# Kernel optimization log

Hardware: AMD Instinct MI355X
Metric: run time of the kernel (lower is better)

The kernel has to match this reference:

```python
import jax, jax.numpy as jnp
import numpy as np

B, S, DIM = 2, 2048, 4096
HQ, HKV, HD = 32, 8, 128
N_REP = HQ // HKV
MAX_S = 2048
ROPE_BASE = 10000.0


def rotate_half(x):
    half = x.shape[-1] // 2
    return jnp.concatenate([-x[..., half:], x[..., :half]], axis=-1)


def setup_inputs() -> dict:
    key = jax.random.key(0)
    ks = jax.random.split(key, 8)
    x = jax.random.normal(ks[0], (B, S, DIM), dtype=jnp.float32)
    Wq = jax.random.normal(ks[1], (HQ * HD, DIM), dtype=jnp.float32) * 0.02
    bq = jax.random.normal(ks[2], (HQ * HD,), dtype=jnp.float32) * 0.02
    Wk = jax.random.normal(ks[3], (HKV * HD, DIM), dtype=jnp.float32) * 0.02
    bk = jax.random.normal(ks[4], (HKV * HD,), dtype=jnp.float32) * 0.02
    Wv = jax.random.normal(ks[5], (HKV * HD, DIM), dtype=jnp.float32) * 0.02
    bv = jax.random.normal(ks[6], (HKV * HD,), dtype=jnp.float32) * 0.02
    Wo = jax.random.normal(ks[7], (DIM, HQ * HD), dtype=jnp.float32) * 0.02
    # RoPE tables (HF convention: angles duplicated across both halves)
    inv_freq = 1.0 / (ROPE_BASE ** (jnp.arange(0, HD, 2, dtype=jnp.float32) / HD))
    pos = jnp.arange(S, dtype=jnp.float32)
    ang = pos[:, None] * inv_freq[None, :]              # [S, HD/2]
    emb = jnp.concatenate([ang, ang], axis=-1)          # [S, HD]
    cos, sin = jnp.cos(emb), jnp.sin(emb)
    # static KV cache, zero-initialized as in the module
    cache_k = jnp.zeros((B, HKV, MAX_S, HD), dtype=jnp.float32)
    cache_v = jnp.zeros((B, HKV, MAX_S, HD), dtype=jnp.float32)
    # causal additive mask
    causal = jnp.tril(jnp.ones((S, S), dtype=bool))
    mask = jnp.where(causal, 0.0, -1e9).astype(jnp.float32)[None, None]  # [1,1,S,S]
    return {"x": x, "cos": cos, "sin": sin, "Wq": Wq, "bq": bq, "Wk": Wk,
            "bk": bk, "Wv": Wv, "bv": bv, "Wo": Wo, "cache_k": cache_k,
            "cache_v": cache_v, "mask": mask, "start_pos": 0}


def reference(x, cos, sin, Wq, bq, Wk, bk, Wv, bv, Wo, cache_k, cache_v, mask, start_pos):
    bsz, seqlen, _ = x.shape
    scaling = 1.0 / jnp.sqrt(jnp.float32(HD))
    # QKV projections
    xq = (jnp.einsum('bsd,ed->bse', x, Wq) + bq).reshape(bsz, seqlen, HQ, HD).transpose(0, 2, 1, 3)
    xk = (jnp.einsum('bsd,ed->bse', x, Wk) + bk).reshape(bsz, seqlen, HKV, HD).transpose(0, 2, 1, 3)
    xv = (jnp.einsum('bsd,ed->bse', x, Wv) + bv).reshape(bsz, seqlen, HKV, HD).transpose(0, 2, 1, 3)
    # RoPE
    c = cos[None, None]  # [1,1,S,HD]
    s = sin[None, None]
    xq = xq * c + rotate_half(xq) * s
    xk = xk * c + rotate_half(xk) * s
    # static KV-cache append + slice (start_pos is a Python int)
    cache_k = jax.lax.dynamic_update_slice(cache_k, xk, (0, 0, start_pos, 0))
    cache_v = jax.lax.dynamic_update_slice(cache_v, xv, (0, 0, start_pos, 0))
    keys = cache_k[:, :, :start_pos + seqlen]     # [B,HKV,K,HD]
    values = cache_v[:, :, :start_pos + seqlen]
    # GQA: repeat kv heads (repeat_interleave over head dim)
    keys = jnp.repeat(keys, N_REP, axis=1)        # [B,HQ,K,HD]
    values = jnp.repeat(values, N_REP, axis=1)
    # SDPA with additive mask
    scores = jnp.einsum('bhqd,bhkd->bhqk', xq, keys) * scaling + mask
    attn = jax.nn.softmax(scores, axis=-1)
    out = jnp.einsum('bhqk,bhkd->bhqd', attn, values)
    out = out.transpose(0, 2, 1, 3).reshape(bsz, seqlen, HQ * HD)
    return jnp.einsum('bse,de->bsd', out, Wo)
```

## Files before the change

### kernel.cpp

```cpp
#include <hip/hip_runtime.h>

typedef _Float16 half8 __attribute__((ext_vector_type(8)));
typedef _Float16 half4 __attribute__((ext_vector_type(4)));
typedef float floatx4 __attribute__((ext_vector_type(4)));
typedef float floatx16 __attribute__((ext_vector_type(16)));

#define SWZ(r) ((((r) & 7) << 1) | (((r) >> 3) & 1))

__device__ __forceinline__ void gld16(const void* g, void* l) {
  __builtin_amdgcn_global_load_lds(
      (const __attribute__((address_space(1))) unsigned int*)g,
      (__attribute__((address_space(3))) unsigned int*)l, 16, 0, 0);
}

__global__ void convert_all(const float* __restrict__ x, const float* __restrict__ Wq,
                            const float* __restrict__ Wk, const float* __restrict__ Wv,
                            const float* __restrict__ Wo, const float* __restrict__ bq,
                            const float* __restrict__ bk, const float* __restrict__ bv,
                            _Float16* __restrict__ xb, _Float16* __restrict__ wqkv,
                            _Float16* __restrict__ wo_b, float* __restrict__ biasc) {
  long i = (long)blockIdx.x * 256 + threadIdx.x;
  const long N0 = 2097152, N1 = N0 + 2097152, N2 = N1 + 524288, N3 = N2 + 524288,
             N4 = N3 + 2097152;
  const float* s;
  _Float16* d;
  long j;
  if (i < N0) { s = x; d = xb; j = i; }
  else if (i < N1) { s = Wq; d = wqkv; j = i - N0; }
  else if (i < N2) { s = Wk; d = wqkv + (size_t)4096 * 4096; j = i - N1; }
  else if (i < N3) { s = Wv; d = wqkv + (size_t)5120 * 4096; j = i - N2; }
  else if (i < N4) { s = Wo; d = wo_b; j = i - N3; }
  else {
    long k = i - N4;
    if (k < 4096) biasc[k] = bq[k];
    else if (k < 5120) biasc[k] = bk[k - 4096];
    else if (k < 6144) biasc[k] = bv[k - 5120];
    return;
  }
  float4 a = ((const float4*)s)[2 * j];
  float4 b2 = ((const float4*)s)[2 * j + 1];
  half8 h;
  h[0] = (_Float16)a.x; h[1] = (_Float16)a.y; h[2] = (_Float16)a.z; h[3] = (_Float16)a.w;
  h[4] = (_Float16)b2.x; h[5] = (_Float16)b2.y; h[6] = (_Float16)b2.z; h[7] = (_Float16)b2.w;
  ((half8*)d)[j] = h;
}

template <typename OutT, bool HasBias>
__global__ __launch_bounds__(256) void gemm_bt(const _Float16* __restrict__ A,
                                               const _Float16* __restrict__ B,
                                               const float* __restrict__ bias,
                                               OutT* __restrict__ C, int M, int N, int K) {
  __shared__ _Float16 as[128 * 64];
  __shared__ _Float16 bs[128 * 64];
  const int tid = threadIdx.x;
  const int w = tid >> 6, lane = tid & 63;
  const int quad = lane >> 4, l16 = lane & 15;
  const int M0 = blockIdx.y * 128, N0 = blockIdx.x * 128;
  const int wm = (w >> 1) * 64, wn = (w & 1) * 64;

  floatx4 acc[4][4];
#pragma unroll
  for (int i = 0; i < 4; ++i)
#pragma unroll
    for (int j = 0; j < 4; ++j) acc[i][j] = (floatx4){0.f, 0.f, 0.f, 0.f};

  const int sr = tid >> 3, g0 = tid & 7;
  const int csw = (g0 ^ (sr & 7)) * 8;
  const _Float16* Ag[4];
  const _Float16* Bg[4];
  _Float16* asd[4];
  _Float16* bsd[4];
#pragma unroll
  for (int c = 0; c < 4; ++c) {
    Ag[c] = A + (size_t)(M0 + c * 32 + sr) * K + csw;
    Bg[c] = B + (size_t)(N0 + c * 32 + sr) * K + csw;
    asd[c] = &as[(c * 32 + w * 8) * 64];
    bsd[c] = &bs[(c * 32 + w * 8) * 64];
  }

  int aoff[4][2], boff[4][2];
#pragma unroll
  for (int mi = 0; mi < 4; ++mi)
#pragma unroll
    for (int kd = 0; kd < 2; ++kd) {
      int ra = wm + mi * 16 + l16;
      aoff[mi][kd] = ra * 64 + (((kd * 4 + quad) ^ (ra & 7)) * 8);
      int rb = wn + mi * 16 + l16;
      boff[mi][kd] = rb * 64 + (((kd * 4 + quad) ^ (rb & 7)) * 8);
    }

  for (int kk = 0; kk < K; kk += 64) {
    __syncthreads();
#pragma unroll
    for (int c = 0; c < 4; ++c) gld16(Ag[c] + kk, asd[c]);
#pragma unroll
    for (int c = 0; c < 4; ++c) gld16(Bg[c] + kk, bsd[c]);
    __syncthreads();
#pragma unroll
    for (int kd = 0; kd < 2; ++kd) {
      half8 af[4], bf[4];
#pragma unroll
      for (int i = 0; i < 4; ++i) af[i] = *(const half8*)&as[aoff[i][kd]];
#pragma unroll
      for (int i = 0; i < 4; ++i) bf[i] = *(const half8*)&bs[boff[i][kd]];
#pragma unroll
      for (int mi = 0; mi < 4; ++mi)
#pragma unroll
        for (int ni = 0; ni < 4; ++ni)
          acc[mi][ni] = __builtin_amdgcn_mfma_f32_16x16x32_f16(af[mi], bf[ni], acc[mi][ni], 0, 0, 0);
    }
  }

#pragma unroll
  for (int mi = 0; mi < 4; ++mi)
#pragma unroll
    for (int ni = 0; ni < 4; ++ni) {
      int row = M0 + wm + mi * 16 + quad * 4;
      int col = N0 + wn + ni * 16 + l16;
      float bvv = HasBias ? bias[col] : 0.f;
#pragma unroll
      for (int r = 0; r < 4; ++r) {
        float v = acc[mi][ni][r] + bvv;
        C[(size_t)(row + r) * N + col] = (OutT)v;
      }
    }
}

template <typename OutT, bool HasBias>
__global__ __launch_bounds__(512, 2) void gemm256(const _Float16* __restrict__ A,
                                                  const _Float16* __restrict__ B,
                                                  const float* __restrict__ bias,
                                                  OutT* __restrict__ C, int M, int N, int K) {
  __shared__ _Float16 as[2][256 * 64];
  __shared__ _Float16 bs[2][256 * 64];
  const int tid = threadIdx.x;
  const int w = tid >> 6, lane = tid & 63;
  const int quad = lane >> 4, l16 = lane & 15;
  const int sw7 = l16 & 7;
  const int M0 = blockIdx.y * 256, N0 = blockIdx.x * 256;
  const int wm = (w >> 2) * 128, wn = (w & 3) * 64;
  const int NT = K >> 6;

  floatx4 acc[8][4];
#pragma unroll
  for (int i = 0; i < 8; ++i)
#pragma unroll
    for (int j = 0; j < 4; ++j) acc[i][j] = (floatx4){0.f, 0.f, 0.f, 0.f};

  const int sr = tid >> 3;
  const int csw = ((tid & 7) ^ (sr & 7)) * 8;
  const _Float16* Ag[4];
  const _Float16* Bg[4];
#pragma unroll
  for (int j = 0; j < 4; ++j) {
    Ag[j] = A + (size_t)(M0 + j * 64 + sr) * K + csw;
    Bg[j] = B + (size_t)(N0 + j * 64 + sr) * K + csw;
  }

#define STA(p, t, j) gld16(Ag[j] + (size_t)(t) * 64, &as[p][(j) * 4096 + w * 512])
#define STB(p, t, j) gld16(Bg[j] + (size_t)(t) * 64, &bs[p][(j) * 4096 + w * 512])

#define FRA(p, q, mi, kd) \
  (*(const half8*)&as[p][(wm + (q) * 32 + (mi) * 16 + l16) * 64 + ((((kd) * 4 + quad) ^ sw7) * 8)])
#define FRB(p, ni, kd) \
  (*(const half8*)&bs[p][(wn + (ni) * 16 + l16) * 64 + ((((kd) * 4 + quad) ^ sw7) * 8)])

#define LD_A(p, q)                                   \
  _Pragma("unroll") for (int kd = 0; kd < 2; ++kd)   \
  _Pragma("unroll") for (int mi = 0; mi < 2; ++mi)   \
      af[mi][kd] = FRA(p, q, mi, kd);

#define LD_B(p)                                      \
  _Pragma("unroll") for (int kd = 0; kd < 2; ++kd)   \
  _Pragma("unroll") for (int ni = 0; ni < 4; ++ni)   \
      bf[ni][kd] = FRB(p, ni, kd);

#define PH_COMPUTE(q)                                                                  \
  __builtin_amdgcn_s_barrier();                                                        \
  asm volatile("s_waitcnt lgkmcnt(0)" ::: "memory");                                   \
  __builtin_amdgcn_sched_barrier(0);                                                   \
  __builtin_amdgcn_s_setprio(1);                                                       \
  _Pragma("unroll") for (int kd = 0; kd < 2; ++kd)                                     \
  _Pragma("unroll") for (int mi = 0; mi < 2; ++mi)                                     \
  _Pragma("unroll") for (int ni = 0; ni < 4; ++ni)                                     \
      acc[(q) * 2 + mi][ni] = __builtin_amdgcn_mfma_f32_16x16x32_f16(                  \
          af[mi][kd], bf[ni][kd], acc[(q) * 2 + mi][ni], 0, 0, 0);                     \
  __builtin_amdgcn_s_setprio(0);

  half8 bf[4][2], af[2][2];

  STA(0, 0, 0); STA(0, 0, 1); STA(0, 0, 2); STA(0, 0, 3);
  STB(0, 0, 0); STB(0, 0, 1); STB(0, 0, 2); STB(0, 0, 3);
  STB(1, 1, 0); STB(1, 1, 1); STB(1, 1, 2); STB(1, 1, 3);
  asm volatile("s_waitcnt vmcnt(4)" ::: "memory");
  __builtin_amdgcn_s_barrier();

  for (int t = 0; t < NT; t += 2) {
    const int t2 = (t + 2 < NT) ? t + 2 : t;
    const int t3 = (t + 3 < NT) ? t + 3 : t + 1;

    LD_B(0); LD_A(0, 0);
    STA(1, t + 1, 0); STA(1, t + 1, 1); STA(1, t + 1, 2); STA(1, t + 1, 3);
    PH_COMPUTE(0);
    __builtin_amdgcn_s_barrier();

    LD_A(0, 1);
    STB(0, t2, 0); STB(0, t2, 1);
    PH_COMPUTE(1);
    __builtin_amdgcn_s_barrier();

    LD_A(0, 2);
    STB(0, t2, 2); STB(0, t2, 3);
    PH_COMPUTE(2);
    __builtin_amdgcn_s_barrier();

    LD_A(0, 3);
    PH_COMPUTE(3);
    asm volatile("s_waitcnt vmcnt(4)" ::: "memory");
    __builtin_amdgcn_sched_barrier(0);
    __builtin_amdgcn_s_barrier();

    LD_B(1); LD_A(1, 0);
    STA(0, t2, 0); STA(0, t2, 1);
    PH_COMPUTE(0);
    __builtin_amdgcn_s_barrier();

    LD_A(1, 1);
    STA(0, t2, 2); STA(0, t2, 3);
    PH_COMPUTE(1);
    __builtin_amdgcn_s_barrier();

    LD_A(1, 2);
    STB(1, t3, 0); STB(1, t3, 1);
    PH_COMPUTE(2);
    __builtin_amdgcn_s_barrier();

    LD_A(1, 3);
    STB(1, t3, 2); STB(1, t3, 3);
    PH_COMPUTE(3);
    asm volatile("s_waitcnt vmcnt(4)" ::: "memory");
    __builtin_amdgcn_sched_barrier(0);
    __builtin_amdgcn_s_barrier();
  }
  asm volatile("s_waitcnt vmcnt(0)" ::: "memory");

#pragma unroll
  for (int mf = 0; mf < 8; ++mf)
#pragma unroll
    for (int ni = 0; ni < 4; ++ni) {
      int row = M0 + wm + mf * 16 + quad * 4;
      int col = N0 + wn + ni * 16 + l16;
      float bvv = HasBias ? bias[col] : 0.f;
#pragma unroll
      for (int r = 0; r < 4; ++r) C[(size_t)(row + r) * N + col] = (OutT)(acc[mf][ni][r] + bvv);
    }
#undef STA
#undef STB
#undef FRA
#undef FRB
#undef LD_A
#undef LD_B
#undef PH_COMPUTE
}

__global__ void rope_qk(const _Float16* __restrict__ qkv, const float* __restrict__ cosb,
                        const float* __restrict__ sinb, _Float16* __restrict__ q_r,
                        _Float16* __restrict__ k_r) {
  int t = blockIdx.x * 256 + threadIdx.x;
  int d = t & 63;
  int r = t >> 6;
  int hh = r % 40;
  int r2 = r / 40;
  int s = r2 & 2047;
  int b = r2 >> 11;
  size_t mrow = (size_t)(b * 2048 + s) * 6144;
  float c = cosb[s * 128 + d], sn = sinb[s * 128 + d];
  if (hh < 32) {
    size_t base = mrow + hh * 128 + d;
    float x1 = (float)qkv[base], x2 = (float)qkv[base + 64];
    const float sc = 0.12751744737079736f;
    float o1 = (x1 * c - x2 * sn) * sc;
    float o2 = (x2 * c + x1 * sn) * sc;
    size_t ob = ((size_t)((b * 32 + hh) * 2048 + s)) * 128 + d;
    q_r[ob] = (_Float16)o1;
    q_r[ob + 64] = (_Float16)o2;
  } else {
    int hk = hh - 32;
    size_t base = mrow + 4096 + hk * 128 + d;
    float x1 = (float)qkv[base], x2 = (float)qkv[base + 64];
    float o1 = x1 * c - x2 * sn;
    float o2 = x2 * c + x1 * sn;
    size_t ob = ((size_t)((b * 8 + hk) * 2048 + s)) * 128 + d;
    k_r[ob] = (_Float16)o1;
    k_r[ob + 64] = (_Float16)o2;
  }
}

__global__ void v_transpose(const _Float16* __restrict__ qkv, _Float16* __restrict__ v_t) {
  __shared__ _Float16 tile[32][33];
  int st = blockIdx.x * 32, dt = blockIdx.y * 32, bh = blockIdx.z;
  int tx = threadIdx.x & 31, ty = threadIdx.x >> 5;
  int b = bh >> 3, hv = bh & 7;
#pragma unroll
  for (int j = 0; j < 4; ++j) {
    int s = st + ty + j * 8;
    tile[ty + j * 8][tx] = qkv[(size_t)(b * 2048 + s) * 6144 + 5120 + hv * 128 + dt + tx];
  }
  __syncthreads();
#pragma unroll
  for (int j = 0; j < 4; ++j)
    v_t[((size_t)bh * 128 + dt + ty + j * 8) * 2048 + st + tx] = tile[tx][ty + j * 8];
}

__global__ __launch_bounds__(256, 2) void attn_kernel(const _Float16* __restrict__ q_r,
                                                      const _Float16* __restrict__ k_r,
                                                      const _Float16* __restrict__ v_t,
                                                      _Float16* __restrict__ att) {
  __shared__ __align__(16) _Float16 kbuf[2][64 * 128];
  __shared__ __align__(16) _Float16 vbuf[2][128 * 64];
  const int tid = threadIdx.x;
  const int w = tid >> 6, lane = tid & 63;
  const int l32 = lane & 31, hi = lane >> 5;
  const int qb = 15 - blockIdx.x;
  const int h = blockIdx.y, b = blockIdx.z;
  const int q0 = qb * 128;
  const _Float16* qh = q_r + ((size_t)(b * 32 + h) * 2048) * 128;
  const _Float16* kh = k_r + ((size_t)(b * 8 + (h >> 2)) * 2048) * 128;
  const _Float16* vh = v_t + ((size_t)(b * 8 + (h >> 2)) * 128) * 2048;

  const int ql = w * 32 + l32;
  const int myq = q0 + ql;
  const int swq7 = ql & 7;
  const int swl = SWZ(l32);

  half8 bq[8];
#pragma unroll
  for (int kd = 0; kd < 8; ++kd)
    bq[kd] = *(const half8*)&qh[(size_t)myq * 128 + kd * 16 + hi * 8];

  floatx16 oacc[4];
#pragma unroll
  for (int di = 0; di < 4; ++di)
#pragma unroll
    for (int j = 0; j < 16; ++j) oacc[di][j] = 0.f;
  float mrun = -1e30f, lrun = 0.f;

  const int krow = tid >> 4, kgrp = tid & 15;
  const int vrow = tid >> 3, vgrp = tid & 7;

#define STAGE_KV(p, t)                                                                     \
  do {                                                                                     \
    const _Float16* kg_ = kh + (size_t)(t) * 64 * 128;                                     \
    _Pragma("unroll") for (int c = 0; c < 4; ++c) {                                        \
      int row = c * 16 + krow;                                                             \
      gld16(kg_ + row * 128 + ((kgrp ^ SWZ(row)) * 8), &kbuf[p][(c * 16 + w * 4) * 128]);  \
    }                                                                                      \
    _Pragma("unroll") for (int c = 0; c < 4; ++c) {                                        \
      int row = c * 32 + vrow;                                                             \
      gld16(vh + (size_t)row * 2048 + (size_t)(t) * 64 + ((vgrp ^ (row & 7)) * 8),         \
            &vbuf[p][(c * 32 + w * 8) * 64]);                                              \
    }                                                                                      \
  } while (0)

  const int nsteps = 2 * qb + 2;
  STAGE_KV(0, 0);

  for (int s = 0; s < nsteps; ++s) {
    const int cur = s & 1;
    __syncthreads();
    const int sn = (s + 1 < nsteps) ? s + 1 : s;
    STAGE_KV(cur ^ 1, sn);
    asm volatile("s_waitcnt vmcnt(8)" ::: "memory");
    __syncthreads();

    floatx16 sacc[2];
#pragma unroll
    for (int ni = 0; ni < 2; ++ni)
#pragma unroll
      for (int j = 0; j < 16; ++j) sacc[ni][j] = 0.f;
#pragma unroll
    for (int ni = 0; ni < 2; ++ni) {
      int rb = (ni * 32 + l32) * 128;
#pragma unroll
      for (int kd = 0; kd < 8; ++kd) {
        half8 ka = *(const half8*)&kbuf[cur][rb + (((kd * 2 + hi) ^ swl) * 8)];
        sacc[ni] = __builtin_amdgcn_mfma_f32_32x32x16_f16(ka, bq[kd], sacc[ni], 0, 0, 0);
      }
    }

    if (s >= 2 * qb) {
      int kv0 = s * 64;
#pragma unroll
      for (int ni = 0; ni < 2; ++ni)
#pragma unroll
        for (int g = 0; g < 4; ++g) {
          int kvb = kv0 + ni * 32 + g * 8 + hi * 4;
#pragma unroll
          for (int t = 0; t < 4; ++t)
            if (kvb + t > myq) sacc[ni][g * 4 + t] = -1e30f;
        }
    }

    float tm = -1e30f;
#pragma unroll
    for (int ni = 0; ni < 2; ++ni)
#pragma unroll
      for (int j = 0; j < 16; ++j) tm = fmaxf(tm, sacc[ni][j]);
    tm = fmaxf(tm, __shfl_xor(tm, 32));
    float nm = fmaxf(mrun, tm);
    float al = exp2f(mrun - nm);
    mrun = nm;
    float ts = 0.f;
#pragma unroll
    for (int ni = 0; ni < 2; ++ni)
#pragma unroll
      for (int j = 0; j < 16; ++j) {
        float p = exp2f(sacc[ni][j] - nm);
        sacc[ni][j] = p;
        ts += p;
      }
    ts += __shfl_xor(ts, 32);
    lrun = lrun * al + ts;
#pragma unroll
    for (int di = 0; di < 4; ++di)
#pragma unroll
      for (int j = 0; j < 16; ++j) oacc[di][j] *= al;

    __syncthreads();

#pragma unroll
    for (int ni = 0; ni < 2; ++ni)
#pragma unroll
      for (int g = 0; g < 4; ++g) {
        half4 p4;
#pragma unroll
        for (int t = 0; t < 4; ++t) p4[t] = (_Float16)sacc[ni][g * 4 + t];
        *(half4*)&kbuf[cur][ql * 64 + (((ni * 4 + g) ^ swq7) * 8) + hi * 4] = p4;
      }

#pragma unroll
    for (int ks = 0; ks < 4; ++ks) {
      half8 pb = *(const half8*)&kbuf[cur][ql * 64 + (((ks * 2 + hi) ^ swq7) * 8)];
#pragma unroll
      for (int di = 0; di < 4; ++di) {
        int rv = (di * 32 + l32) * 64;
        half8 va = *(const half8*)&vbuf[cur][rv + (((ks * 2 + hi) ^ (l32 & 7)) * 8)];
        oacc[di] = __builtin_amdgcn_mfma_f32_32x32x16_f16(va, pb, oacc[di], 0, 0, 0);
      }
    }
  }
  asm volatile("s_waitcnt vmcnt(0)" ::: "memory");

  float inv = 1.f / lrun;
  _Float16* ob = att + ((size_t)b * 2048 + myq) * 4096 + h * 128;
#pragma unroll
  for (int di = 0; di < 4; ++di)
#pragma unroll
    for (int g = 0; g < 4; ++g) {
      half4 o4;
#pragma unroll
      for (int t = 0; t < 4; ++t) o4[t] = (_Float16)(oacc[di][g * 4 + t] * inv);
      *(half4*)&ob[di * 32 + g * 8 + hi * 4] = o4;
    }
#undef STAGE_KV
}

extern "C" void kernel_launch(void* const* d_in, const int* in_sizes, int n_in, void* d_out,
                              int out_size, void* d_ws, size_t ws_size, hipStream_t stream) {
  const float* x = (const float*)d_in[0];
  const float* cosb = (const float*)d_in[1];
  const float* sinb = (const float*)d_in[2];
  const float* Wq = (const float*)d_in[3];
  const float* bq = (const float*)d_in[4];
  const float* Wk = (const float*)d_in[5];
  const float* bk = (const float*)d_in[6];
  const float* Wv = (const float*)d_in[7];
  const float* bv = (const float*)d_in[8];
  const float* Wo = (const float*)d_in[9];
  float* out = (float*)d_out;

  char* p = (char*)d_ws;
  _Float16* xb = (_Float16*)p;   p += (size_t)4096 * 4096 * 2;
  _Float16* wqkv = (_Float16*)p; p += (size_t)6144 * 4096 * 2;
  _Float16* wo_b = (_Float16*)p; p += (size_t)4096 * 4096 * 2;
  _Float16* qkv = (_Float16*)p;  p += (size_t)4096 * 6144 * 2;
  _Float16* q_r = (_Float16*)p;  p += (size_t)2 * 32 * 2048 * 128 * 2;
  _Float16* k_r = (_Float16*)p;  p += (size_t)2 * 8 * 2048 * 128 * 2;
  _Float16* v_t = (_Float16*)p;  p += (size_t)2 * 8 * 128 * 2048 * 2;
  _Float16* att = (_Float16*)p;  p += (size_t)4096 * 4096 * 2;
  float* biasc = (float*)p;      p += 6144 * 4;

  convert_all<<<28696, 256, 0, stream>>>(x, Wq, Wk, Wv, Wo, bq, bk, bv, xb, wqkv, wo_b, biasc);

  gemm_bt<_Float16, true><<<dim3(48, 32), 256, 0, stream>>>(xb, wqkv, biasc, qkv, 4096, 6144, 4096);
  rope_qk<<<40960, 256, 0, stream>>>(qkv, cosb, sinb, q_r, k_r);
  v_transpose<<<dim3(64, 4, 16), 256, 0, stream>>>(qkv, v_t);
  attn_kernel<<<dim3(16, 32, 2), 256, 0, stream>>>(q_r, k_r, v_t, att);
  gemm256<float, false><<<dim3(16, 16), 512, 0, stream>>>(att, wo_b, nullptr, out, 4096, 4096, 4096);
}
```

Before: 881.2 us.

## Fuse RoPE and V transpose into the QKV GEMM epilogue

The QKV projection GEMM now stages its 128x128 output tile in shared memory and, per head, applies RoPE with the query scaling for Q/K heads or writes the transposed V layout directly. This removes the intermediate qkv buffer round trip through global memory and two separate kernel launches. In exchange it adds an epilogue with extra shared-memory traffic and syncs, larger shared memory per block, and strided 4-byte stores for the V transpose.

```diff
diff --git a/kernel.cpp b/kernel.cpp
--- a/kernel.cpp
+++ b/kernel.cpp
@@ -2,6 +2,7 @@
 
 typedef _Float16 half8 __attribute__((ext_vector_type(8)));
 typedef _Float16 half4 __attribute__((ext_vector_type(4)));
+typedef _Float16 half2v __attribute__((ext_vector_type(2)));
 typedef float floatx4 __attribute__((ext_vector_type(4)));
 typedef float floatx16 __attribute__((ext_vector_type(16)));
 
@@ -45,13 +46,14 @@
   ((half8*)d)[j] = h;
 }
 
-template <typename OutT, bool HasBias>
-__global__ __launch_bounds__(256) void gemm_bt(const _Float16* __restrict__ A,
-                                               const _Float16* __restrict__ B,
-                                               const float* __restrict__ bias,
-                                               OutT* __restrict__ C, int M, int N, int K) {
-  __shared__ _Float16 as[128 * 64];
-  __shared__ _Float16 bs[128 * 64];
+__global__ __launch_bounds__(256) void gemm_qkv_fused(
+    const _Float16* __restrict__ A, const _Float16* __restrict__ B,
+    const float* __restrict__ bias, const float* __restrict__ cosb,
+    const float* __restrict__ sinb, _Float16* __restrict__ q_r,
+    _Float16* __restrict__ k_r, _Float16* __restrict__ v_t, int M, int N, int K) {
+  __shared__ _Float16 smem[128 * 130];
+  _Float16* as = smem;
+  _Float16* bs = smem + 128 * 64;
   const int tid = threadIdx.x;
   const int w = tid >> 6, lane = tid & 63;
   const int quad = lane >> 4, l16 = lane & 15;
@@ -111,19 +113,64 @@
     }
   }
 
+  __syncthreads();
 #pragma unroll
   for (int mi = 0; mi < 4; ++mi)
 #pragma unroll
     for (int ni = 0; ni < 4; ++ni) {
-      int row = M0 + wm + mi * 16 + quad * 4;
-      int col = N0 + wn + ni * 16 + l16;
-      float bvv = HasBias ? bias[col] : 0.f;
+      int col = wn + ni * 16 + l16;
+      float bvv = bias[N0 + col];
 #pragma unroll
       for (int r = 0; r < 4; ++r) {
-        float v = acc[mi][ni][r] + bvv;
-        C[(size_t)(row + r) * N + col] = (OutT)v;
-      }
-    }
+        int row = wm + mi * 16 + quad * 4 + r;
+        smem[row * 130 + col] = (_Float16)(acc[mi][ni][r] + bvv);
+      }
+    }
+  __syncthreads();
+
+  const int hh = blockIdx.x;
+  const int bb = M0 >> 11;
+  const int sl0 = M0 & 2047;
+
+  if (hh < 40) {
+    _Float16* base = (hh < 32)
+        ? q_r + ((size_t)(bb * 32 + hh) * 2048 + sl0) * 128
+        : k_r + ((size_t)(bb * 8 + (hh - 32)) * 2048 + sl0) * 128;
+    const float sc = (hh < 32) ? 0.12751744737079736f : 1.0f;
+    const int d4 = (tid & 15) * 4, r0 = tid >> 4;
+#pragma unroll
+    for (int pp = 0; pp < 8; ++pp) {
+      int row = r0 + pp * 16;
+      int sl = sl0 + row;
+      float4 cc = *(const float4*)&cosb[sl * 128 + d4];
+      float4 ss = *(const float4*)&sinb[sl * 128 + d4];
+      half4 x1 = *(const half4*)&smem[row * 130 + d4];
+      half4 x2 = *(const half4*)&smem[row * 130 + d4 + 64];
+      const float* cf = (const float*)&cc;
+      const float* sf = (const float*)&ss;
+      half4 o1, o2;
+#pragma unroll
+      for (int i = 0; i < 4; ++i) {
+        float xx1 = (float)x1[i], xx2 = (float)x2[i];
+        o1[i] = (_Float16)((xx1 * cf[i] - xx2 * sf[i]) * sc);
+        o2[i] = (_Float16)((xx2 * cf[i] + xx1 * sf[i]) * sc);
+      }
+      *(half4*)&base[(size_t)row * 128 + d4] = o1;
+      *(half4*)&base[(size_t)row * 128 + d4 + 64] = o2;
+    }
+  } else {
+    const int hv = hh - 40;
+    _Float16* vb = v_t + (size_t)(bb * 8 + hv) * 128 * 2048 + sl0;
+    const int d0 = tid >> 6, sp = (tid & 63) * 2;
+#pragma unroll
+    for (int pp = 0; pp < 32; ++pp) {
+      int d = d0 + pp * 4;
+      half2v o;
+      o[0] = smem[sp * 130 + d];
+      o[1] = smem[(sp + 1) * 130 + d];
+      *(half2v*)&vb[(size_t)d * 2048 + sp] = o;
+    }
+  }
 }
 
 template <typename OutT, bool HasBias>
@@ -261,55 +308,6 @@
 #undef LD_A
 #undef LD_B
 #undef PH_COMPUTE
-}
-
-__global__ void rope_qk(const _Float16* __restrict__ qkv, const float* __restrict__ cosb,
-                        const float* __restrict__ sinb, _Float16* __restrict__ q_r,
-                        _Float16* __restrict__ k_r) {
-  int t = blockIdx.x * 256 + threadIdx.x;
-  int d = t & 63;
-  int r = t >> 6;
-  int hh = r % 40;
-  int r2 = r / 40;
-  int s = r2 & 2047;
-  int b = r2 >> 11;
-  size_t mrow = (size_t)(b * 2048 + s) * 6144;
-  float c = cosb[s * 128 + d], sn = sinb[s * 128 + d];
-  if (hh < 32) {
-    size_t base = mrow + hh * 128 + d;
-    float x1 = (float)qkv[base], x2 = (float)qkv[base + 64];
-    const float sc = 0.12751744737079736f;
-    float o1 = (x1 * c - x2 * sn) * sc;
-    float o2 = (x2 * c + x1 * sn) * sc;
-    size_t ob = ((size_t)((b * 32 + hh) * 2048 + s)) * 128 + d;
-    q_r[ob] = (_Float16)o1;
-    q_r[ob + 64] = (_Float16)o2;
-  } else {
-    int hk = hh - 32;
-    size_t base = mrow + 4096 + hk * 128 + d;
-    float x1 = (float)qkv[base], x2 = (float)qkv[base + 64];
-    float o1 = x1 * c - x2 * sn;
-    float o2 = x2 * c + x1 * sn;
-    size_t ob = ((size_t)((b * 8 + hk) * 2048 + s)) * 128 + d;
-    k_r[ob] = (_Float16)o1;
-    k_r[ob + 64] = (_Float16)o2;
-  }
-}
-
-__global__ void v_transpose(const _Float16* __restrict__ qkv, _Float16* __restrict__ v_t) {
-  __shared__ _Float16 tile[32][33];
-  int st = blockIdx.x * 32, dt = blockIdx.y * 32, bh = blockIdx.z;
-  int tx = threadIdx.x & 31, ty = threadIdx.x >> 5;
-  int b = bh >> 3, hv = bh & 7;
-#pragma unroll
-  for (int j = 0; j < 4; ++j) {
-    int s = st + ty + j * 8;
-    tile[ty + j * 8][tx] = qkv[(size_t)(b * 2048 + s) * 6144 + 5120 + hv * 128 + dt + tx];
-  }
-  __syncthreads();
-#pragma unroll
-  for (int j = 0; j < 4; ++j)
-    v_t[((size_t)bh * 128 + dt + ty + j * 8) * 2048 + st + tx] = tile[tx][ty + j * 8];
 }
 
 __global__ __launch_bounds__(256, 2) void attn_kernel(const _Float16* __restrict__ q_r,
@@ -483,7 +481,6 @@
   _Float16* xb = (_Float16*)p;   p += (size_t)4096 * 4096 * 2;
   _Float16* wqkv = (_Float16*)p; p += (size_t)6144 * 4096 * 2;
   _Float16* wo_b = (_Float16*)p; p += (size_t)4096 * 4096 * 2;
-  _Float16* qkv = (_Float16*)p;  p += (size_t)4096 * 6144 * 2;
   _Float16* q_r = (_Float16*)p;  p += (size_t)2 * 32 * 2048 * 128 * 2;
   _Float16* k_r = (_Float16*)p;  p += (size_t)2 * 8 * 2048 * 128 * 2;
   _Float16* v_t = (_Float16*)p;  p += (size_t)2 * 8 * 128 * 2048 * 2;
@@ -492,9 +489,8 @@
 
   convert_all<<<28696, 256, 0, stream>>>(x, Wq, Wk, Wv, Wo, bq, bk, bv, xb, wqkv, wo_b, biasc);
 
-  gemm_bt<_Float16, true><<<dim3(48, 32), 256, 0, stream>>>(xb, wqkv, biasc, qkv, 4096, 6144, 4096);
-  rope_qk<<<40960, 256, 0, stream>>>(qkv, cosb, sinb, q_r, k_r);
-  v_transpose<<<dim3(64, 4, 16), 256, 0, stream>>>(qkv, v_t);
+  gemm_qkv_fused<<<dim3(48, 32), 256, 0, stream>>>(xb, wqkv, biasc, cosb, sinb, q_r, k_r, v_t,
+                                                   4096, 6144, 4096);
   attn_kernel<<<dim3(16, 32, 2), 256, 0, stream>>>(q_r, k_r, v_t, att);
   gemm256<float, false><<<dim3(16, 16), 512, 0, stream>>>(att, wo_b, nullptr, out, 4096, 4096, 4096);
 }
```

Measured after the change: 833.4 us. 1.06x faster.
